# Kernel optimization log

Hardware: AMD Instinct MI355X
Metric: run time of the kernel (lower is better)

The kernel has to match this reference:

```python
import jax, jax.numpy as jnp
import numpy as np

N = 1_000_000          # total nodes (polyline points)
PTS_PER_CLUSTER = 20
C = N // PTS_PER_CLUSTER  # 50_000 clusters (polylines)
B = 32                 # graphs in batch
IN_F, HID, OUT_F, NUM_LAYERS = 16, 64, 128, 3
EPS_LN = 1e-5


def _mlp(x, w1, b1, g, be, w2, b2):
    # Linear -> LayerNorm -> ReLU -> Linear
    h = x @ w1 + b1
    mu = jnp.mean(h, axis=-1, keepdims=True)
    var = jnp.var(h, axis=-1, keepdims=True)
    h = (h - mu) * jax.lax.rsqrt(var + EPS_LN) * g + be
    h = jax.nn.relu(h)
    return h @ w2 + b2


def setup_inputs() -> dict:
    key = jax.random.key(0)
    ks = iter(jax.random.split(key, 64))

    def lin(k, fi, fo):
        s = 1.0 / np.sqrt(fi)
        return jax.random.uniform(k, (fi, fo), jnp.float32, -s, s)

    x = jax.random.normal(next(ks), (N, IN_F), jnp.float32)
    clusters = (jnp.arange(N) // PTS_PER_CLUSTER).astype(jnp.int64)  # sorted, each cluster has 20 pts
    batch = ((clusters * B) // C).astype(jnp.int64)                  # consistent graph ids

    inp = {"x": x, "clusters": clusters, "batch": batch}
    # pre MLP: IN_F -> HID -> HID
    inp.update(pre_w1=lin(next(ks), IN_F, HID), pre_b1=jnp.zeros((HID,), jnp.float32),
               pre_g=jnp.ones((HID,), jnp.float32), pre_be=jnp.zeros((HID,), jnp.float32),
               pre_w2=lin(next(ks), HID, HID), pre_b2=jnp.zeros((HID,), jnp.float32))
    # subgraph layers: HID -> HID -> HID//2 (concat with pooled -> HID)
    for i in range(NUM_LAYERS):
        inp[f"l{i}_w1"] = lin(next(ks), HID, HID)
        inp[f"l{i}_b1"] = jnp.zeros((HID,), jnp.float32)
        inp[f"l{i}_g"] = jnp.ones((HID,), jnp.float32)
        inp[f"l{i}_be"] = jnp.zeros((HID,), jnp.float32)
        inp[f"l{i}_w2"] = lin(next(ks), HID, HID // 2)
        inp[f"l{i}_b2"] = jnp.zeros((HID // 2,), jnp.float32)
    # output MLP: HID -> HID -> OUT_F
    inp.update(out_w1=lin(next(ks), HID, HID), out_b1=jnp.zeros((HID,), jnp.float32),
               out_g=jnp.ones((HID,), jnp.float32), out_be=jnp.zeros((HID,), jnp.float32),
               out_w2=lin(next(ks), HID, OUT_F), out_b2=jnp.zeros((OUT_F,), jnp.float32))
    return inp


def reference(x, clusters, batch,
              pre_w1, pre_b1, pre_g, pre_be, pre_w2, pre_b2,
              l0_w1, l0_b1, l0_g, l0_be, l0_w2, l0_b2,
              l1_w1, l1_b1, l1_g, l1_be, l1_w2, l1_b2,
              l2_w1, l2_b1, l2_g, l2_be, l2_w2, l2_b2,
              out_w1, out_b1, out_g, out_be, out_w2, out_b2):
    x = x.astype(jnp.float32)
    out = _mlp(x, pre_w1, pre_b1, pre_g, pre_be, pre_w2, pre_b2)  # [N, HID]
    layer_params = [(l0_w1, l0_b1, l0_g, l0_be, l0_w2, l0_b2),
                    (l1_w1, l1_b1, l1_g, l1_be, l1_w2, l1_b2),
                    (l2_w1, l2_b1, l2_g, l2_be, l2_w2, l2_b2)]
    for p in layer_params:
        h = _mlp(out, *p)                                          # [N, HID/2]
        pooled = jax.ops.segment_max(h, clusters, num_segments=C)  # [C, HID/2] scatter-max
        out = jnp.concatenate([h, pooled[clusters]], axis=-1)      # [N, HID]
    # max_pool_x: per-cluster feature max + per-cluster batch id
    out = jax.ops.segment_max(out, clusters, num_segments=C)       # [C, HID]
    batch_out = jax.ops.segment_max(batch, clusters, num_segments=C)
    out = _mlp(out, out_w1, out_b1, out_g, out_be, out_w2, out_b2)  # [C, OUT_F]
    norm = jnp.linalg.norm(out, ord=2, axis=-1, keepdims=True)
    out = out / jnp.maximum(norm, 1e-12)
    return out, batch_out
```

## Files before the change

kernel.cpp:

```cpp
#include <hip/hip_runtime.h>


#define ASTR 72

typedef short v8s __attribute__((ext_vector_type(8)));
typedef float v4f __attribute__((ext_vector_type(4)));

#define MFMA __builtin_amdgcn_mfma_f32_16x16x32_bf16

#define OFF_PW1 0
#define OFF_FB  2048
#define OFF_LW1(L) (6144 + (L) * 6144)
#define OFF_LW2(L) (OFF_LW1(L) + 4096)
#define OFF_OW1 24576
#define OFF_OW2 28672

__device__ __forceinline__ short bfb(float v) {
  __bf16 b = (__bf16)v;
  return __builtin_bit_cast(short, b);
}

__global__ void kT(const float* __restrict__ pw1, const float* __restrict__ pw2,
                   const float* __restrict__ w1a, const float* __restrict__ w2a,
                   const float* __restrict__ w1b, const float* __restrict__ w2b,
                   const float* __restrict__ w1c, const float* __restrict__ w2c,
                   const float* __restrict__ ow1, const float* __restrict__ ow2,
                   const float* __restrict__ pb2, const float* __restrict__ b1a,
                   short* __restrict__ ws) {
  if (blockIdx.x == 1) {
    float* fb = (float*)(ws + OFF_FB);
    for (int f = threadIdx.x; f < 64; f += blockDim.x) {
      float s = b1a[f];
      for (int m = 0; m < 64; ++m) s = fmaf(pb2[m], w1a[m * 64 + f], s);
      fb[f] = s;
    }
    return;
  }
  if (blockIdx.x == 2) {
    const int off = OFF_LW1(0);
    const int total = 64 * 8;
    for (int i = threadIdx.x; i < total; i += blockDim.x) {
      const int f = i % 64;
      const int kq = i / 64;
      v8s h;
#pragma unroll
      for (int j = 0; j < 8; ++j) {
        const int k = kq * 8 + j;
        float s = 0.f;
        for (int m = 0; m < 64; ++m) s = fmaf(pw2[k * 64 + m], w1a[m * 64 + f], s);
        h[j] = bfb(s);
      }
      *(v8s*)(ws + off + f * 64 + kq * 8) = h;
    }
    return;
  }
  const float* W; int K, F, Kpad, off;
  switch (blockIdx.x) {
    case 0: W = pw1; K = 16; F = 64;  Kpad = 32; off = OFF_PW1; break;
    case 3: W = w2a; K = 64; F = 32;  Kpad = 64; off = OFF_LW2(0); break;
    case 4: W = w1b; K = 64; F = 64;  Kpad = 64; off = OFF_LW1(1); break;
    case 5: W = w2b; K = 64; F = 32;  Kpad = 64; off = OFF_LW2(1); break;
    case 6: W = w1c; K = 64; F = 64;  Kpad = 64; off = OFF_LW1(2); break;
    case 7: W = w2c; K = 64; F = 32;  Kpad = 64; off = OFF_LW2(2); break;
    case 8: W = ow1; K = 64; F = 64;  Kpad = 64; off = OFF_OW1; break;
    default: W = ow2; K = 64; F = 128; Kpad = 64; off = OFF_OW2; break;
  }
  const int total = F * (Kpad >> 3);
  for (int i = threadIdx.x; i < total; i += blockDim.x) {
    const int f = i % F;
    const int kq = i / F;
    v8s h;
#pragma unroll
    for (int j = 0; j < 8; ++j) {
      const int k = kq * 8 + j;
      h[j] = bfb((k < K) ? W[k * F + f] : 0.f);
    }
    *(v8s*)(ws + off + f * Kpad + kq * 8) = h;
  }
}

template <int NT, int KS>
__device__ __forceinline__ void mmT(const short* A, int tb, const v8s* Wf,
                                    const v4f* bias4, int col, int quad,
                                    v4f* acc) {
#pragma unroll
  for (int t = 0; t < NT; ++t) acc[t] = bias4[t];
#pragma unroll
  for (int ks = 0; ks < KS; ++ks) {
    const v8s b = *(const v8s*)(A + (tb + col) * ASTR + ks * 32 + quad * 8);
#pragma unroll
    for (int t = 0; t < NT; ++t)
      acc[t] = MFMA(Wf[t * KS + ks], b, acc[t], 0, 0, 0);
  }
}

template <int NT>
__device__ __forceinline__ void mmT_split(const short* A, int tb,
                                          const v8s* Wf, const v4f* bias4,
                                          int col, int quad, v4f* acc) {
  const int node = tb + col;
  const int cl = (node * 205) >> 12;
  const v8s b0 = *(const v8s*)(A + node * ASTR + quad * 8);
  const v8s b1 = *(const v8s*)(A + (cl * 4 + quad) * ASTR + 64);
#pragma unroll
  for (int t = 0; t < NT; ++t) {
    v4f a = bias4[t];
    a = MFMA(Wf[t * 2 + 0], b0, a, 0, 0, 0);
    a = MFMA(Wf[t * 2 + 1], b1, a, 0, 0, 0);
    acc[t] = a;
  }
}

__device__ __forceinline__ void lnT_write(short* Aw, int tb, int col, int quad,
                                          v4f* acc, const v4f* g4,
                                          const v4f* be4) {
  float mu = 0.f, sq = 0.f;
#pragma unroll
  for (int t = 0; t < 4; ++t)
#pragma unroll
    for (int r = 0; r < 4; ++r) {
      mu += acc[t][r];
      sq = fmaf(acc[t][r], acc[t][r], sq);
    }
  mu += __shfl_xor(mu, 16); mu += __shfl_xor(mu, 32);
  sq += __shfl_xor(sq, 16); sq += __shfl_xor(sq, 32);
  mu *= (1.0f / 64.0f);
  const float var = sq * (1.0f / 64.0f) - mu * mu;
  const float rs = rsqrtf(var + 1e-5f);
#pragma unroll
  for (int t = 0; t < 4; ++t) {
    short4 s;
#pragma unroll
    for (int r = 0; r < 4; ++r) {
      float v = fmaf((acc[t][r] - mu) * rs, g4[t][r], be4[t][r]);
      ((short*)&s)[r] = bfb(fmaxf(v, 0.f));
    }
    *(short4*)(Aw + (tb + col) * ASTR + t * 16 + quad * 4) = s;
  }
}

template <int NT>
__device__ __forceinline__ void plainT_write(short* Aw, int tb, int col,
                                             int quad, v4f* acc) {
#pragma unroll
  for (int t = 0; t < NT; ++t) {
    short4 s;
#pragma unroll
    for (int r = 0; r < 4; ++r) ((short*)&s)[r] = bfb(acc[t][r]);
    *(short4*)(Aw + (tb + col) * ASTR + t * 16 + quad * 4) = s;
  }
}

__global__ void __launch_bounds__(128, 2)
kF(const float* __restrict__ x, const int* __restrict__ batch,
   const short* __restrict__ wsW,
   const float* __restrict__ pb1, const float* __restrict__ pg,
   const float* __restrict__ pbe,
   const float* __restrict__ b1a, const float* __restrict__ ga,
   const float* __restrict__ bea, const float* __restrict__ b2a,
   const float* __restrict__ b1b, const float* __restrict__ gb,
   const float* __restrict__ beb, const float* __restrict__ b2b,
   const float* __restrict__ b1c, const float* __restrict__ gc_,
   const float* __restrict__ bec, const float* __restrict__ b2c,
   const float* __restrict__ ob1, const float* __restrict__ og,
   const float* __restrict__ obe, const float* __restrict__ ob2,
   float* __restrict__ out, int C) {
  __shared__ __align__(16) short act[2 * 80 * ASTR];
  const int tid = threadIdx.x;
  const int lane = tid & 63;
  const int wave = tid >> 6;
  const int col = lane & 15;
  const int quad = lane >> 4;
  const int cbase = blockIdx.x * 8 + wave * 4;
  if (cbase >= C) return;
  const int nc = min(4, C - cbase);
  const int nrows = nc * 20;
  const int ntiles = (nrows + 15) >> 4;
  short* A = act + wave * 80 * ASTR;

  {
    v8s Wf[4]; v4f b4[4], g4[4], be4[4];
#pragma unroll
    for (int t = 0; t < 4; ++t) {
      Wf[t] = *(const v8s*)(wsW + OFF_PW1 + (t * 16 + col) * 32 + quad * 8);
      b4[t]  = *(const v4f*)(pb1 + t * 16 + quad * 4);
      g4[t]  = *(const v4f*)(pg  + t * 16 + quad * 4);
      be4[t] = *(const v4f*)(pbe + t * 16 + quad * 4);
    }
    const float4* x4 = (const float4*)x;
    const long nb = (long)cbase * 20;
    for (int T = 0; T < ntiles; ++T) {
      const int node = T * 16 + col;
      v8s b = {0, 0, 0, 0, 0, 0, 0, 0};
      if (quad < 2 && node < nrows) {
        const float4 v0 = x4[(nb + node) * 4 + quad * 2];
        const float4 v1 = x4[(nb + node) * 4 + quad * 2 + 1];
        b[0] = bfb(v0.x); b[1] = bfb(v0.y); b[2] = bfb(v0.z); b[3] = bfb(v0.w);
        b[4] = bfb(v1.x); b[5] = bfb(v1.y); b[6] = bfb(v1.z); b[7] = bfb(v1.w);
      }
      v4f acc[4];
#pragma unroll
      for (int t = 0; t < 4; ++t) acc[t] = MFMA(Wf[t], b, b4[t], 0, 0, 0);
      lnT_write(A, T * 16, col, quad, acc, g4, be4);
    }
  }


  const float* fb = (const float*)(wsW + OFF_FB);
  const float* B1p[3] = {fb, b1b, b1c};
  const float* Gp[3]  = {ga, gb, gc_};
  const float* BEp[3] = {bea, beb, bec};
  const float* B2p[3] = {b2a, b2b, b2c};

  for (int L = 0; L < 3; ++L) {
    v8s W1f[8], W2f[4];
    v4f b14[4], g4[4], be4[4], b24[2];
    const short* w1 = wsW + OFF_LW1(L);
    const short* w2 = wsW + OFF_LW2(L);
#pragma unroll
    for (int t = 0; t < 4; ++t) {
#pragma unroll
      for (int ks = 0; ks < 2; ++ks)
        W1f[t * 2 + ks] = *(const v8s*)(w1 + (t * 16 + col) * 64 + ks * 32 + quad * 8);
      b14[t] = *(const v4f*)(B1p[L] + t * 16 + quad * 4);
      g4[t]  = *(const v4f*)(Gp[L]  + t * 16 + quad * 4);
      be4[t] = *(const v4f*)(BEp[L] + t * 16 + quad * 4);
    }
#pragma unroll
    for (int t = 0; t < 2; ++t) {
#pragma unroll
      for (int ks = 0; ks < 2; ++ks)
        W2f[t * 2 + ks] = *(const v8s*)(w2 + (t * 16 + col) * 64 + ks * 32 + quad * 8);
      b24[t] = *(const v4f*)(B2p[L] + t * 16 + quad * 4);
    }
    for (int T = 0; T < ntiles; ++T) {
      v4f acc[4];
      if (L == 0)
        mmT<4, 2>(A, T * 16, W1f, b14, col, quad, acc);
      else
        mmT_split<4>(A, T * 16, W1f, b14, col, quad, acc);
      lnT_write(A, T * 16, col, quad, acc, g4, be4);
      v4f h[2];
      mmT<2, 2>(A, T * 16, W2f, b24, col, quad, h);
      plainT_write<2>(A, T * 16, col, quad, h);
    }
    {
      const int cl = quad, jp = col;
      if (cl < nc) {
        const uint* AU = (const uint*)A;
        float m0 = -3.4e38f, m1 = -3.4e38f;
#pragma unroll
        for (int r = 0; r < 20; ++r) {
          const uint v = AU[(cl * 20 + r) * (ASTR / 2) + jp];
          m0 = fmaxf(m0, __builtin_bit_cast(float, v << 16));
          m1 = fmaxf(m1, __builtin_bit_cast(float, v & 0xFFFF0000u));
        }
        const uint pv = (uint)(unsigned short)bfb(m0) |
                        ((uint)(unsigned short)bfb(m1) << 16);
        uint* AW = (uint*)A;
        if (L < 2) {
          AW[(cl * 4 + (jp >> 2)) * (ASTR / 2) + 32 + (jp & 3)] = pv;
        } else {
          AW[cl * (ASTR / 2) + jp] = pv;
          AW[cl * (ASTR / 2) + 16 + jp] = pv;
        }
      }
    }
  }

  {
    v8s Wf[8]; v4f b4[4], g4[4], be4[4];
#pragma unroll
    for (int t = 0; t < 4; ++t) {
#pragma unroll
      for (int ks = 0; ks < 2; ++ks)
        Wf[t * 2 + ks] = *(const v8s*)(wsW + OFF_OW1 + (t * 16 + col) * 64 + ks * 32 + quad * 8);
      b4[t]  = *(const v4f*)(ob1 + t * 16 + quad * 4);
      g4[t]  = *(const v4f*)(og  + t * 16 + quad * 4);
      be4[t] = *(const v4f*)(obe + t * 16 + quad * 4);
    }
    v4f acc[4];
    mmT<4, 2>(A, 0, Wf, b4, col, quad, acc);
    lnT_write(A, 0, col, quad, acc, g4, be4);
  }
  {
    v4f acc[8];
    const v8s bb0 = *(const v8s*)(A + col * ASTR + quad * 8);
    const v8s bb1 = *(const v8s*)(A + col * ASTR + 32 + quad * 8);
#pragma unroll
    for (int half = 0; half < 2; ++half) {
      v8s Wf[8];
#pragma unroll
      for (int t = 0; t < 4; ++t)
#pragma unroll
        for (int ks = 0; ks < 2; ++ks)
          Wf[t * 2 + ks] = *(const v8s*)(wsW + OFF_OW2 +
                             ((half * 4 + t) * 16 + col) * 64 + ks * 32 + quad * 8);
#pragma unroll
      for (int t = 0; t < 4; ++t) {
        v4f a = *(const v4f*)(ob2 + (half * 4 + t) * 16 + quad * 4);
        a = MFMA(Wf[t * 2], bb0, a, 0, 0, 0);
        a = MFMA(Wf[t * 2 + 1], bb1, a, 0, 0, 0);
        acc[half * 4 + t] = a;
      }
    }
    float sq = 0.f;
#pragma unroll
    for (int t = 0; t < 8; ++t)
#pragma unroll
      for (int r = 0; r < 4; ++r) sq = fmaf(acc[t][r], acc[t][r], sq);
    sq += __shfl_xor(sq, 16); sq += __shfl_xor(sq, 32);
    const float inv = 1.0f / fmaxf(sqrtf(sq), 1e-12f);
    if (col < nc) {
      const long gcl = cbase + col;
#pragma unroll
      for (int t = 0; t < 8; ++t) {
        float4 v = {acc[t][0] * inv, acc[t][1] * inv,
                    acc[t][2] * inv, acc[t][3] * inv};
        *(float4*)(out + gcl * 128 + t * 16 + quad * 4) = v;
      }
      if (quad == 0) out[(long)C * 128 + gcl] = (float)batch[gcl * 20];
    }
  }
}

extern "C" void kernel_launch(void* const* d_in, const int* in_sizes, int n_in,
                              void* d_out, int out_size, void* d_ws, size_t ws_size,
                              hipStream_t stream) {
  const float* x     = (const float*)d_in[0];
  const int*   batch = (const int*)d_in[2];
  const float* pw1 = (const float*)d_in[3];
  const float* pb1 = (const float*)d_in[4];
  const float* pg  = (const float*)d_in[5];
  const float* pbe = (const float*)d_in[6];
  const float* pw2 = (const float*)d_in[7];
  const float* pb2 = (const float*)d_in[8];
  const float* w1a = (const float*)d_in[9];
  const float* b1a = (const float*)d_in[10];
  const float* ga  = (const float*)d_in[11];
  const float* bea = (const float*)d_in[12];
  const float* w2a = (const float*)d_in[13];
  const float* b2a = (const float*)d_in[14];
  const float* w1b = (const float*)d_in[15];
  const float* b1b = (const float*)d_in[16];
  const float* gb  = (const float*)d_in[17];
  const float* beb = (const float*)d_in[18];
  const float* w2b = (const float*)d_in[19];
  const float* b2b = (const float*)d_in[20];
  const float* w1c = (const float*)d_in[21];
  const float* b1c = (const float*)d_in[22];
  const float* gc  = (const float*)d_in[23];
  const float* bec = (const float*)d_in[24];
  const float* w2c = (const float*)d_in[25];
  const float* b2c = (const float*)d_in[26];
  const float* ow1 = (const float*)d_in[27];
  const float* ob1 = (const float*)d_in[28];
  const float* og  = (const float*)d_in[29];
  const float* obe = (const float*)d_in[30];
  const float* ow2 = (const float*)d_in[31];
  const float* ob2 = (const float*)d_in[32];

  const int N = in_sizes[0] / 16;
  const int C = N / 20;
  short* ws16 = (short*)d_ws;
  float* out = (float*)d_out;

  hipLaunchKernelGGL(kT, dim3(10), dim3(256), 0, stream,
                     pw1, pw2, w1a, w2a, w1b, w2b, w1c, w2c, ow1, ow2,
                     pb2, b1a, ws16);

  const int blocks = (C + 7) / 8;
  hipLaunchKernelGGL(kF, dim3(blocks), dim3(128), 0, stream,
                     x, batch, (const short*)ws16,
                     pb1, pg, pbe,
                     b1a, ga, bea, b2a,
                     b1b, gb, beb, b2b,
                     b1c, gc, bec, b2c,
                     ob1, og, obe, ob2,
                     out, C);
}
```

Baseline: 302.9 us.

## Pool both waves' clusters into shared tile for a single output MLP pass

Each wave used to run the output MLP on its own 4 clusters, so three quarters of every 16-column MFMA tile held padding. Now both waves write their pooled cluster features into a shared 16-row buffer. After a block barrier, wave 0 alone runs the output MLP and normalisation for all 8 clusters, which halves the output-stage MFMA work and weight loads. In exchange it adds a __syncthreads, a little more LDS, and a serial tail where wave 1 sits idle.

```diff
diff --git a/kernel.cpp b/kernel.cpp
--- a/kernel.cpp
+++ b/kernel.cpp
@@ -166,108 +166,121 @@
    const float* __restrict__ obe, const float* __restrict__ ob2,
    float* __restrict__ out, int C) {
   __shared__ __align__(16) short act[2 * 80 * ASTR];
+  __shared__ __align__(16) short outT[16 * ASTR];
   const int tid = threadIdx.x;
   const int lane = tid & 63;
   const int wave = tid >> 6;
   const int col = lane & 15;
   const int quad = lane >> 4;
-  const int cbase = blockIdx.x * 8 + wave * 4;
-  if (cbase >= C) return;
-  const int nc = min(4, C - cbase);
+  const int blockBase = blockIdx.x * 8;
+  if (blockBase >= C) return;
+  const int cbase = blockBase + wave * 4;
+  const int nc = min(4, max(0, C - cbase));
   const int nrows = nc * 20;
   const int ntiles = (nrows + 15) >> 4;
   short* A = act + wave * 80 * ASTR;
 
-  {
-    v8s Wf[4]; v4f b4[4], g4[4], be4[4];
-#pragma unroll
-    for (int t = 0; t < 4; ++t) {
-      Wf[t] = *(const v8s*)(wsW + OFF_PW1 + (t * 16 + col) * 32 + quad * 8);
-      b4[t]  = *(const v4f*)(pb1 + t * 16 + quad * 4);
-      g4[t]  = *(const v4f*)(pg  + t * 16 + quad * 4);
-      be4[t] = *(const v4f*)(pbe + t * 16 + quad * 4);
-    }
-    const float4* x4 = (const float4*)x;
-    const long nb = (long)cbase * 20;
-    for (int T = 0; T < ntiles; ++T) {
-      const int node = T * 16 + col;
-      v8s b = {0, 0, 0, 0, 0, 0, 0, 0};
-      if (quad < 2 && node < nrows) {
-        const float4 v0 = x4[(nb + node) * 4 + quad * 2];
-        const float4 v1 = x4[(nb + node) * 4 + quad * 2 + 1];
-        b[0] = bfb(v0.x); b[1] = bfb(v0.y); b[2] = bfb(v0.z); b[3] = bfb(v0.w);
-        b[4] = bfb(v1.x); b[5] = bfb(v1.y); b[6] = bfb(v1.z); b[7] = bfb(v1.w);
-      }
-      v4f acc[4];
-#pragma unroll
-      for (int t = 0; t < 4; ++t) acc[t] = MFMA(Wf[t], b, b4[t], 0, 0, 0);
-      lnT_write(A, T * 16, col, quad, acc, g4, be4);
-    }
-  }
-
-
-  const float* fb = (const float*)(wsW + OFF_FB);
-  const float* B1p[3] = {fb, b1b, b1c};
-  const float* Gp[3]  = {ga, gb, gc_};
-  const float* BEp[3] = {bea, beb, bec};
-  const float* B2p[3] = {b2a, b2b, b2c};
-
-  for (int L = 0; L < 3; ++L) {
-    v8s W1f[8], W2f[4];
-    v4f b14[4], g4[4], be4[4], b24[2];
-    const short* w1 = wsW + OFF_LW1(L);
-    const short* w2 = wsW + OFF_LW2(L);
-#pragma unroll
-    for (int t = 0; t < 4; ++t) {
-#pragma unroll
-      for (int ks = 0; ks < 2; ++ks)
-        W1f[t * 2 + ks] = *(const v8s*)(w1 + (t * 16 + col) * 64 + ks * 32 + quad * 8);
-      b14[t] = *(const v4f*)(B1p[L] + t * 16 + quad * 4);
-      g4[t]  = *(const v4f*)(Gp[L]  + t * 16 + quad * 4);
-      be4[t] = *(const v4f*)(BEp[L] + t * 16 + quad * 4);
-    }
-#pragma unroll
-    for (int t = 0; t < 2; ++t) {
-#pragma unroll
-      for (int ks = 0; ks < 2; ++ks)
-        W2f[t * 2 + ks] = *(const v8s*)(w2 + (t * 16 + col) * 64 + ks * 32 + quad * 8);
-      b24[t] = *(const v4f*)(B2p[L] + t * 16 + quad * 4);
-    }
-    for (int T = 0; T < ntiles; ++T) {
-      v4f acc[4];
-      if (L == 0)
-        mmT<4, 2>(A, T * 16, W1f, b14, col, quad, acc);
-      else
-        mmT_split<4>(A, T * 16, W1f, b14, col, quad, acc);
-      lnT_write(A, T * 16, col, quad, acc, g4, be4);
-      v4f h[2];
-      mmT<2, 2>(A, T * 16, W2f, b24, col, quad, h);
-      plainT_write<2>(A, T * 16, col, quad, h);
-    }
+  if (wave == 0) {
+    uint* OTu = (uint*)outT;
+    for (int i = lane; i < 288; i += 64) OTu[288 + i] = 0u;
+  }
+
+  if (nc > 0) {
     {
-      const int cl = quad, jp = col;
-      if (cl < nc) {
-        const uint* AU = (const uint*)A;
-        float m0 = -3.4e38f, m1 = -3.4e38f;
-#pragma unroll
-        for (int r = 0; r < 20; ++r) {
-          const uint v = AU[(cl * 20 + r) * (ASTR / 2) + jp];
-          m0 = fmaxf(m0, __builtin_bit_cast(float, v << 16));
-          m1 = fmaxf(m1, __builtin_bit_cast(float, v & 0xFFFF0000u));
+      v8s Wf[4]; v4f b4[4], g4[4], be4[4];
+#pragma unroll
+      for (int t = 0; t < 4; ++t) {
+        Wf[t] = *(const v8s*)(wsW + OFF_PW1 + (t * 16 + col) * 32 + quad * 8);
+        b4[t]  = *(const v4f*)(pb1 + t * 16 + quad * 4);
+        g4[t]  = *(const v4f*)(pg  + t * 16 + quad * 4);
+        be4[t] = *(const v4f*)(pbe + t * 16 + quad * 4);
+      }
+      const float4* x4 = (const float4*)x;
+      const long nb = (long)cbase * 20;
+      for (int T = 0; T < ntiles; ++T) {
+        const int node = T * 16 + col;
+        v8s b = {0, 0, 0, 0, 0, 0, 0, 0};
+        if (quad < 2 && node < nrows) {
+          const float4 v0 = x4[(nb + node) * 4 + quad * 2];
+          const float4 v1 = x4[(nb + node) * 4 + quad * 2 + 1];
+          b[0] = bfb(v0.x); b[1] = bfb(v0.y); b[2] = bfb(v0.z); b[3] = bfb(v0.w);
+          b[4] = bfb(v1.x); b[5] = bfb(v1.y); b[6] = bfb(v1.z); b[7] = bfb(v1.w);
         }
-        const uint pv = (uint)(unsigned short)bfb(m0) |
-                        ((uint)(unsigned short)bfb(m1) << 16);
-        uint* AW = (uint*)A;
-        if (L < 2) {
-          AW[(cl * 4 + (jp >> 2)) * (ASTR / 2) + 32 + (jp & 3)] = pv;
-        } else {
-          AW[cl * (ASTR / 2) + jp] = pv;
-          AW[cl * (ASTR / 2) + 16 + jp] = pv;
+        v4f acc[4];
+#pragma unroll
+        for (int t = 0; t < 4; ++t) acc[t] = MFMA(Wf[t], b, b4[t], 0, 0, 0);
+        lnT_write(A, T * 16, col, quad, acc, g4, be4);
+      }
+    }
+
+    const float* fb = (const float*)(wsW + OFF_FB);
+    const float* B1p[3] = {fb, b1b, b1c};
+    const float* Gp[3]  = {ga, gb, gc_};
+    const float* BEp[3] = {bea, beb, bec};
+    const float* B2p[3] = {b2a, b2b, b2c};
+
+    for (int L = 0; L < 3; ++L) {
+      v8s W1f[8], W2f[4];
+      v4f b14[4], g4[4], be4[4], b24[2];
+      const short* w1 = wsW + OFF_LW1(L);
+      const short* w2 = wsW + OFF_LW2(L);
+#pragma unroll
+      for (int t = 0; t < 4; ++t) {
+#pragma unroll
+        for (int ks = 0; ks < 2; ++ks)
+          W1f[t * 2 + ks] = *(const v8s*)(w1 + (t * 16 + col) * 64 + ks * 32 + quad * 8);
+        b14[t] = *(const v4f*)(B1p[L] + t * 16 + quad * 4);
+        g4[t]  = *(const v4f*)(Gp[L]  + t * 16 + quad * 4);
+        be4[t] = *(const v4f*)(BEp[L] + t * 16 + quad * 4);
+      }
+#pragma unroll
+      for (int t = 0; t < 2; ++t) {
+#pragma unroll
+        for (int ks = 0; ks < 2; ++ks)
+          W2f[t * 2 + ks] = *(const v8s*)(w2 + (t * 16 + col) * 64 + ks * 32 + quad * 8);
+        b24[t] = *(const v4f*)(B2p[L] + t * 16 + quad * 4);
+      }
+      for (int T = 0; T < ntiles; ++T) {
+        v4f acc[4];
+        if (L == 0)
+          mmT<4, 2>(A, T * 16, W1f, b14, col, quad, acc);
+        else
+          mmT_split<4>(A, T * 16, W1f, b14, col, quad, acc);
+        lnT_write(A, T * 16, col, quad, acc, g4, be4);
+        v4f h[2];
+        mmT<2, 2>(A, T * 16, W2f, b24, col, quad, h);
+        plainT_write<2>(A, T * 16, col, quad, h);
+      }
+      {
+        const int cl = quad, jp = col;
+        if (cl < nc) {
+          const uint* AU = (const uint*)A;
+          float m0 = -3.4e38f, m1 = -3.4e38f;
+#pragma unroll
+          for (int r = 0; r < 20; ++r) {
+            const uint v = AU[(cl * 20 + r) * (ASTR / 2) + jp];
+            m0 = fmaxf(m0, __builtin_bit_cast(float, v << 16));
+            m1 = fmaxf(m1, __builtin_bit_cast(float, v & 0xFFFF0000u));
+          }
+          const uint pv = (uint)(unsigned short)bfb(m0) |
+                          ((uint)(unsigned short)bfb(m1) << 16);
+          if (L < 2) {
+            uint* AW = (uint*)A;
+            AW[(cl * 4 + (jp >> 2)) * (ASTR / 2) + 32 + (jp & 3)] = pv;
+          } else {
+            uint* OTu = (uint*)outT;
+            OTu[(wave * 4 + cl) * (ASTR / 2) + jp] = pv;
+            OTu[(wave * 4 + cl) * (ASTR / 2) + 16 + jp] = pv;
+          }
         }
       }
     }
   }
 
+  __syncthreads();
+  if (wave != 0) return;
+
+  const int ncb = min(8, C - blockBase);
   {
     v8s Wf[8]; v4f b4[4], g4[4], be4[4];
 #pragma unroll
@@ -280,13 +293,13 @@
       be4[t] = *(const v4f*)(obe + t * 16 + quad * 4);
     }
     v4f acc[4];
-    mmT<4, 2>(A, 0, Wf, b4, col, quad, acc);
-    lnT_write(A, 0, col, quad, acc, g4, be4);
+    mmT<4, 2>(outT, 0, Wf, b4, col, quad, acc);
+    lnT_write(outT, 0, col, quad, acc, g4, be4);
   }
   {
     v4f acc[8];
-    const v8s bb0 = *(const v8s*)(A + col * ASTR + quad * 8);
-    const v8s bb1 = *(const v8s*)(A + col * ASTR + 32 + quad * 8);
+    const v8s bb0 = *(const v8s*)(outT + col * ASTR + quad * 8);
+    const v8s bb1 = *(const v8s*)(outT + col * ASTR + 32 + quad * 8);
 #pragma unroll
     for (int half = 0; half < 2; ++half) {
       v8s Wf[8];
@@ -311,8 +324,8 @@
       for (int r = 0; r < 4; ++r) sq = fmaf(acc[t][r], acc[t][r], sq);
     sq += __shfl_xor(sq, 16); sq += __shfl_xor(sq, 32);
     const float inv = 1.0f / fmaxf(sqrtf(sq), 1e-12f);
-    if (col < nc) {
-      const long gcl = cbase + col;
+    if (col < ncb) {
+      const long gcl = blockBase + col;
 #pragma unroll
       for (int t = 0; t < 8; ++t) {
         float4 v = {acc[t][0] * inv, acc[t][1] * inv,
```

Result: faster. 282.9 us (-6.6%).
